# Kernel optimization log

Hardware: AMD Instinct MI355X
Metric: run time of the kernel (lower is better)

Reference implementation:

```python
import jax, jax.numpy as jnp
import numpy as np

SR = 44100
N_BINS = 84
BPO = 12
FMIN = 32.7
HOP = 1024


def _config():
    # Static CQT geometry (mirrors ICQT.__init__)
    Q = 1.0 / (2.0 ** (1.0 / BPO) - 1.0)
    freqs = FMIN * 2.0 ** (np.arange(N_BINS) / BPO)
    wlens = np.round(Q * SR / freqs).astype(np.int64)  # per-bin window lengths (ragged)
    return freqs, wlens


def setup_inputs() -> dict:
    key = jax.random.key(0)
    # complex CQT stacked as (nb_samples, nb_channels, n_bins, n_frames, 2)
    X = jax.random.normal(key, (4, 2, N_BINS, 256, 2), dtype=jnp.float32)
    return {"X": X}


def reference(X):
    freqs, wlens = _config()
    max_wl = int(wlens.max())
    nb_s, nb_c, n_bins, n_frames, _ = X.shape
    # default length in ICQT.forward when length is None
    length = (n_frames - 1) * HOP + max_wl

    Xf = X.reshape(-1, n_bins, n_frames, 2)
    c = (Xf[..., 0] + 1j * Xf[..., 1]).astype(jnp.complex64)  # view_as_complex
    B = c.shape[0]

    starts = np.arange(n_frames) * HOP  # static frame start times
    out = jnp.zeros((B, length), jnp.float32)
    norm_np = np.zeros(length, np.float32)  # norm is input-independent -> static numpy

    for k in range(n_bins):  # fixed structural loop over ragged bins
        L = int(wlens[k])
        t = np.arange(L)
        # torch.hann_window(L) (periodic)
        win = (0.5 - 0.5 * np.cos(2.0 * np.pi * t / L)).astype(np.float32)
        omega = 2.0 * np.pi * float(freqs[k]) / SR
        # exp(+1j*omega*t) * window, fused into one basis vector
        basis = jnp.asarray((np.exp(1j * omega * t) * win).astype(np.complex64))
        # frames: (B, n_frames, L) = outer product of per-frame coeff and basis
        frames = c[:, k, :, None] * basis[None, None, :]
        # vectorized overlap-add scatter (duplicate indices accumulate)
        idx = (starts[:, None] + t[None, :]).reshape(-1)  # (n_frames*L,)
        out = out.at[:, idx].add(jnp.real(frames).reshape(B, -1))
        np.add.at(norm_np, idx, np.tile(win * win, n_frames))

    norm = jnp.asarray(np.where(norm_np > 1e-10, norm_np, 1.0).astype(np.float32))
    out = out / norm[None, :]
    return out.reshape(nb_s, nb_c, -1)
```

## Files before the change

kernel.cpp:

```cpp
#include <hip/hip_runtime.h>
#include <hip/hip_fp16.h>
#include <cmath>

#define NBINS   84
#define NFRAMES 256
#define HOP     1024
#define NB      8
#define KP      960
#define KPH     (KP/2)
#define GBLK    278
#define MROWS   (GBLK*NB)
#define MPAD    2240
#define SD      23

#define BM      64
#define BN      32

#define BT_BLOCKS  1920
#define A_BLOCKS   4200
#define S_BLOCKS   184
#define ALL_BLOCKS (BT_BLOCKS + A_BLOCKS + S_BLOCKS)

typedef _Float16 f16x8 __attribute__((ext_vector_type(8)));
typedef float    f32x4 __attribute__((ext_vector_type(4)));

struct alignas(16) CqtArgs {
    unsigned short ct[KP];
    int   wl[NBINS];
    float omega[NBINS];
    float invL[NBINS];
    int   Ktot;
};

__global__ __launch_bounds__(256)
void build_all(unsigned short* __restrict__ Am, unsigned short* __restrict__ Bt,
               float* __restrict__ S, const float2* __restrict__ X2, CqtArgs a) {
    const int blk = blockIdx.x;
    const int tid = threadIdx.x;
    const float TWOPI = 6.28318530717958647692f;

    if (blk < BT_BLOCKS) {
        const int idx = blk * 256 + tid;
        const int r   = idx / KPH;
        const int j   = idx - r * KPH;
        unsigned int pack = 0;
        const unsigned short rec = a.ct[2 * j];
        if (rec != 0xFFFFu) {
            const int k = rec & 0x7F, d = (rec >> 7) & 0x1F;
            const int t = (d << 10) + r;
            if (t < a.wl[k]) {
                const float tf = (float)t;
                const float w  = 0.5f - 0.5f * cosf(TWOPI * tf * a.invL[k]);
                float s, c;
                sincosf(a.omega[k] * tf, &s, &c);
                pack = (unsigned int)__half_as_ushort(__float2half(c * w))
                     | ((unsigned int)__half_as_ushort(__float2half(s * w)) << 16);
            }
        }
        *(unsigned int*)(Bt + (size_t)r * KP + 2 * j) = pack;
    } else if (blk < BT_BLOCKS + A_BLOCKS) {
        const int idx = (blk - BT_BLOCKS) * 256 + tid;
        const int row = idx / KPH;
        const int j   = idx - row * KPH;
        unsigned int pack = 0;
        const unsigned short rec = a.ct[2 * j];
        if (row < MROWS && rec != 0xFFFFu) {
            const int k = rec & 0x7F, d = (rec >> 7) & 0x1F;
            const int g = row >> 3, b = row & 7;
            const int f = g - d;
            if (f >= 0 && f < NFRAMES) {
                const float2 x = X2[((size_t)b * NBINS + k) * NFRAMES + f];
                pack = (unsigned int)__half_as_ushort(__float2half(x.x))
                     | ((unsigned int)__half_as_ushort(__float2half(-x.y)) << 16);
            }
        }
        *(unsigned int*)(Am + (size_t)row * KP + 2 * j) = pack;
    } else {
        const int gid = (blk - BT_BLOCKS - A_BLOCKS) * 256 + tid;
        const int t   = gid >> 1;
        const int h   = gid & 1;
        float sum = 0.f;
        const int k0 = h * (NBINS / 2);
        for (int k = k0; k < k0 + NBINS / 2; ++k) {
            if (t >= a.wl[k]) break;
            const float w = 0.5f - 0.5f * cosf(TWOPI * (float)t * a.invL[k]);
            sum += w * w;
        }
        const float tot = sum + __shfl_xor(sum, 1, 64);
        if (h == 0) S[t] = tot;
    }
}

__device__ __forceinline__ float inv_norm(const float* __restrict__ S, int g, int ncol) {
    if (g >= GBLK) return 1.0f;
    const int lo = (g > NFRAMES - 1) ? (g - (NFRAMES - 1)) : 0;
    const int hi = g < (SD - 1) ? g : (SD - 1);
    float s = 0.f;
#pragma unroll
    for (int d = 0; d < SD; ++d) {
        const float v = S[(d << 10) + ncol];
        s += (d >= lo && d <= hi) ? v : 0.0f;
    }
    return (s > 1e-10f) ? 1.0f / s : 1.0f;
}

__global__ __launch_bounds__(256)
void gemm_icqt(const unsigned short* __restrict__ Am, const unsigned short* __restrict__ Bt,
               const float* __restrict__ S, float* __restrict__ out, int length) {
    __shared__ __align__(16) char lds[12288];
    const int tid = threadIdx.x;
    const int l   = tid & 63;
    const int wid = tid >> 6;
    const int wm  = wid >> 1, wn = wid & 1;
    const int bm  = blockIdx.x, bn = blockIdx.y;

    const int q0 = tid,      q1 = tid + 256;
    const int r0 = q0 >> 3,  c0 = q0 & 7, s0 = c0 ^ (r0 & 7);
    const int r1 = q1 >> 3,  c1 = q1 & 7, s1 = c1 ^ (r1 & 7);
    const int r2 = tid >> 3, c2 = tid & 7, s2 = c2 ^ (r2 & 7);

    const char* gA0 = (const char*)Am + ((size_t)(bm * BM + r0) * KP + s0 * 8) * 2;
    const char* gA1 = (const char*)Am + ((size_t)(bm * BM + r1) * KP + s1 * 8) * 2;
    const char* gB0 = (const char*)Bt + ((size_t)(bn * BN + r2) * KP + s2 * 8) * 2;
    char* lA = lds;
    char* lB = lds + 8192;

    f32x4 acc0 = {0.f,0.f,0.f,0.f}, acc1 = {0.f,0.f,0.f,0.f};

    f16x8 ra0 = *(const f16x8*)(gA0);
    f16x8 ra1 = *(const f16x8*)(gA1);
    f16x8 rb  = *(const f16x8*)(gB0);

    const int arow0 = wm * 32 + (l & 15), arow1 = arow0 + 16;
    const int brow  = wn * 16 + (l & 15);
    const int kq = l >> 4;

    for (int kk = 0; kk < KP; kk += 64) {
        __syncthreads();
        *(f16x8*)(lA + q0 * 16) = ra0;
        *(f16x8*)(lA + q1 * 16) = ra1;
        *(f16x8*)(lB + tid * 16) = rb;
        __syncthreads();
        if (kk + 64 < KP) {
            ra0 = *(const f16x8*)(gA0 + (kk + 64) * 2);
            ra1 = *(const f16x8*)(gA1 + (kk + 64) * 2);
            rb  = *(const f16x8*)(gB0 + (kk + 64) * 2);
        }
#pragma unroll
        for (int ks = 0; ks < 2; ++ks) {
            const int kb = ks * 4 + kq;
            f16x8 a0 = *(const f16x8*)(lA + arow0 * 128 + ((kb ^ (arow0 & 7)) << 4));
            f16x8 a1 = *(const f16x8*)(lA + arow1 * 128 + ((kb ^ (arow1 & 7)) << 4));
            f16x8 b0 = *(const f16x8*)(lB + brow  * 128 + ((kb ^ (brow  & 7)) << 4));
            acc0 = __builtin_amdgcn_mfma_f32_16x16x32_f16(a0, b0, acc0, 0, 0, 0);
            acc1 = __builtin_amdgcn_mfma_f32_16x16x32_f16(a1, b0, acc1, 0, 0, 0);
        }
    }

    const int mbase = bm * BM + wm * 32;
    const int ncol  = bn * BN + wn * 16 + (l & 15);
    const int g0    = (mbase >> 3) + (kq >> 1);
    const float inv0 = inv_norm(S, g0,     ncol);
    const float inv1 = inv_norm(S, g0 + 2, ncol);

#pragma unroll
    for (int mi = 0; mi < 2; ++mi) {
        const f32x4 v    = mi ? acc1 : acc0;
        const float invv = mi ? inv1 : inv0;
#pragma unroll
        for (int reg = 0; reg < 4; ++reg) {
            const int mrow = mbase + mi * 16 + kq * 4 + reg;
            if (mrow < MROWS) {
                const int g = mrow >> 3, b = mrow & 7;
                const int p = (g << 10) + ncol;
                if (p < length)
                    out[(size_t)b * length + p] = v[reg] * invv;
            }
        }
    }
}

__global__ void icqt_gather_fallback(const float* __restrict__ X, float* __restrict__ out,
                                     CqtArgs a, int length) {
    const int p = blockIdx.x * blockDim.x + threadIdx.x;
    if (p >= length) return;
    float acc[NB];
#pragma unroll
    for (int b = 0; b < NB; ++b) acc[b] = 0.0f;
    float nrm = 0.0f;
    int fhi = p >> 10;
    if (fhi > NFRAMES - 1) fhi = NFRAMES - 1;
    const float2* X2 = reinterpret_cast<const float2*>(X);
    for (int k = 0; k < NBINS; ++k) {
        const int L = a.wl[k];
        int flo = (p - L + HOP) >> 10;
        if (flo < 0) flo = 0;
        for (int f = flo; f <= fhi; ++f) {
            const int t = p - (f << 10);
            if (t < L) {
                float tf = (float)t;
                float ang = a.omega[k] * tf;
                float s = sinf(ang), c = cosf(ang);
                float w = 0.5f - 0.5f * cosf(6.28318530717958647692f * tf * a.invL[k]);
                float bre = c * w, bim = s * w;
                nrm += w * w;
                const int base = k * NFRAMES + f;
#pragma unroll
                for (int b = 0; b < NB; ++b) {
                    float2 cv = X2[(size_t)b * (NBINS * NFRAMES) + base];
                    acc[b] += cv.x * bre - cv.y * bim;
                }
            }
        }
    }
    const float inv = 1.0f / ((nrm > 1e-10f) ? nrm : 1.0f);
#pragma unroll
    for (int b = 0; b < NB; ++b)
        out[(size_t)b * length + p] = acc[b] * inv;
}

extern "C" void kernel_launch(void* const* d_in, const int* in_sizes, int n_in,
                              void* d_out, int out_size, void* d_ws, size_t ws_size,
                              hipStream_t stream) {
    CqtArgs a;
    int cb[NBINS];
    const double SR = 44100.0;
    const double Q  = 1.0 / (std::exp2(1.0 / 12.0) - 1.0);
    int Ktot = 0;
    for (int k = 0; k < NBINS; ++k) {
        double f = 32.7 * std::exp2((double)k / 12.0);
        int L = (int)std::nearbyint(Q * SR / f);
        a.wl[k]    = L;
        cb[k]      = Ktot;
        a.omega[k] = (float)(2.0 * 3.14159265358979323846 * f / SR);
        a.invL[k]  = (float)(1.0 / (double)L);
        Ktot += 2 * ((L + 1023) / 1024);
    }
    a.Ktot = Ktot;
    for (int col = 0; col < KP; ++col) a.ct[col] = 0xFFFF;
    if (Ktot <= KP) {
        for (int k = 0; k < NBINS; ++k) {
            const int D2 = 2 * ((a.wl[k] + 1023) / 1024);
            for (int j = 0; j < D2; ++j)
                a.ct[cb[k] + j] = (unsigned short)(k | ((j >> 1) << 7) | ((j & 1) << 12));
        }
    }

    const int length = out_size / NB;
    const float* X = (const float*)d_in[0];
    float* out     = (float*)d_out;

    const size_t offA = 0;
    const size_t szA  = (size_t)MPAD * KP * 2;
    const size_t offB = offA + szA;
    const size_t szB  = (size_t)1024 * KP * 2;
    const size_t offS = offB + szB;
    const size_t szS  = (size_t)SD * 1024 * 4;
    const size_t need = offS + szS;

    if (Ktot > KP || a.wl[0] > SD * 1024 || ws_size < need) {
        const int blocks = (length + 255) / 256;
        icqt_gather_fallback<<<blocks, 256, 0, stream>>>(X, out, a, length);
        return;
    }

    unsigned short* Am = (unsigned short*)((char*)d_ws + offA);
    unsigned short* Bt = (unsigned short*)((char*)d_ws + offB);
    float*          S  = (float*)((char*)d_ws + offS);

    build_all<<<dim3(ALL_BLOCKS), 256, 0, stream>>>(Am, Bt, S, (const float2*)X, a);
    gemm_icqt<<<dim3(MPAD / BM, 1024 / BN), 256, 0, stream>>>(Am, Bt, S, out, length);
}
```

Before: 47.06 us.

## Double-buffer GEMM K-loop with direct global-to-LDS loads and swizzled block order

Replaces the register-staged single LDS buffer in the GEMM with two LDS buffers filled by global_load_lds instructions, using vmcnt waits and raw barriers so the next K-tile load overlaps the MFMA work. It also flattens the 2D grid into a 1D grid and remaps block IDs so neighbouring blocks share tiles, aiming for better L2 reuse. The LDS footprint doubles, which may lower occupancy. The hand-placed waitcnt and barrier ordering is fragile, and it relies on the direct-to-LDS writes landing in the same XOR-swizzled layout as before.

```diff
diff --git a/kernel.cpp b/kernel.cpp
--- a/kernel.cpp
+++ b/kernel.cpp
@@ -15,6 +15,8 @@
 
 #define BM      64
 #define BN      32
+#define NT      (KP/64)
+#define TILEB   12288
 
 #define BT_BLOCKS  1920
 #define A_BLOCKS   4200
@@ -23,6 +25,14 @@
 
 typedef _Float16 f16x8 __attribute__((ext_vector_type(8)));
 typedef float    f32x4 __attribute__((ext_vector_type(4)));
+
+#define VMCNT(N) asm volatile("s_waitcnt vmcnt(" #N ")" ::: "memory")
+
+__device__ __forceinline__ void gload_lds16(const void* g, void* l) {
+    __builtin_amdgcn_global_load_lds(
+        (__attribute__((address_space(1))) void*)(g),
+        (__attribute__((address_space(3))) void*)(l), 16, 0, 0);
+}
 
 struct alignas(16) CqtArgs {
     unsigned short ct[KP];
@@ -107,12 +117,16 @@
 __global__ __launch_bounds__(256)
 void gemm_icqt(const unsigned short* __restrict__ Am, const unsigned short* __restrict__ Bt,
                const float* __restrict__ S, float* __restrict__ out, int length) {
-    __shared__ __align__(16) char lds[12288];
+    __shared__ __align__(16) char lds[2 * TILEB];
     const int tid = threadIdx.x;
     const int l   = tid & 63;
     const int wid = tid >> 6;
     const int wm  = wid >> 1, wn = wid & 1;
-    const int bm  = blockIdx.x, bn = blockIdx.y;
+
+    const int bid = blockIdx.x;
+    const int swz = (bid & 7) * 140 + (bid >> 3);
+    const int bm  = swz >> 5;
+    const int bn  = swz & 31;
 
     const int q0 = tid,      q1 = tid + 256;
     const int r0 = q0 >> 3,  c0 = q0 & 7, s0 = c0 ^ (r0 & 7);
@@ -122,38 +136,45 @@
     const char* gA0 = (const char*)Am + ((size_t)(bm * BM + r0) * KP + s0 * 8) * 2;
     const char* gA1 = (const char*)Am + ((size_t)(bm * BM + r1) * KP + s1 * 8) * 2;
     const char* gB0 = (const char*)Bt + ((size_t)(bn * BN + r2) * KP + s2 * 8) * 2;
-    char* lA = lds;
-    char* lB = lds + 8192;
 
     f32x4 acc0 = {0.f,0.f,0.f,0.f}, acc1 = {0.f,0.f,0.f,0.f};
-
-    f16x8 ra0 = *(const f16x8*)(gA0);
-    f16x8 ra1 = *(const f16x8*)(gA1);
-    f16x8 rb  = *(const f16x8*)(gB0);
 
     const int arow0 = wm * 32 + (l & 15), arow1 = arow0 + 16;
     const int brow  = wn * 16 + (l & 15);
     const int kq = l >> 4;
 
-    for (int kk = 0; kk < KP; kk += 64) {
-        __syncthreads();
-        *(f16x8*)(lA + q0 * 16) = ra0;
-        *(f16x8*)(lA + q1 * 16) = ra1;
-        *(f16x8*)(lB + tid * 16) = rb;
-        __syncthreads();
-        if (kk + 64 < KP) {
-            ra0 = *(const f16x8*)(gA0 + (kk + 64) * 2);
-            ra1 = *(const f16x8*)(gA1 + (kk + 64) * 2);
-            rb  = *(const f16x8*)(gB0 + (kk + 64) * 2);
-        }
+    {
+        char* bA = lds;            char* bB = lds + 8192;
+        gload_lds16(gA0,       bA + tid * 16);
+        gload_lds16(gA1,       bA + 4096 + tid * 16);
+        gload_lds16(gB0,       bB + tid * 16);
+        char* cA = lds + TILEB;    char* cB = cA + 8192;
+        gload_lds16(gA0 + 128, cA + tid * 16);
+        gload_lds16(gA1 + 128, cA + 4096 + tid * 16);
+        gload_lds16(gB0 + 128, cB + tid * 16);
+    }
+
+#pragma unroll
+    for (int t = 0; t < NT; ++t) {
+        char* bA = lds + (t & 1) * TILEB;
+        char* bB = bA + 8192;
+        if (t + 1 < NT) { VMCNT(3); } else { VMCNT(0); }
+        __builtin_amdgcn_s_barrier();
 #pragma unroll
         for (int ks = 0; ks < 2; ++ks) {
             const int kb = ks * 4 + kq;
-            f16x8 a0 = *(const f16x8*)(lA + arow0 * 128 + ((kb ^ (arow0 & 7)) << 4));
-            f16x8 a1 = *(const f16x8*)(lA + arow1 * 128 + ((kb ^ (arow1 & 7)) << 4));
-            f16x8 b0 = *(const f16x8*)(lB + brow  * 128 + ((kb ^ (brow  & 7)) << 4));
+            f16x8 a0 = *(const f16x8*)(bA + arow0 * 128 + ((kb ^ (arow0 & 7)) << 4));
+            f16x8 a1 = *(const f16x8*)(bA + arow1 * 128 + ((kb ^ (arow1 & 7)) << 4));
+            f16x8 b0 = *(const f16x8*)(bB + brow  * 128 + ((kb ^ (brow  & 7)) << 4));
             acc0 = __builtin_amdgcn_mfma_f32_16x16x32_f16(a0, b0, acc0, 0, 0, 0);
             acc1 = __builtin_amdgcn_mfma_f32_16x16x32_f16(a1, b0, acc1, 0, 0, 0);
+        }
+        if (t + 2 < NT) {
+            __builtin_amdgcn_s_barrier();
+            const int off = (t + 2) * 128;
+            gload_lds16(gA0 + off, bA + tid * 16);
+            gload_lds16(gA1 + off, bA + 4096 + tid * 16);
+            gload_lds16(gB0 + off, bB + tid * 16);
         }
     }
 
@@ -269,5 +290,5 @@
     float*          S  = (float*)((char*)d_ws + offS);
 
     build_all<<<dim3(ALL_BLOCKS), 256, 0, stream>>>(Am, Bt, S, (const float2*)X, a);
-    gemm_icqt<<<dim3(MPAD / BM, 1024 / BN), 256, 0, stream>>>(Am, Bt, S, out, length);
-}
+    gemm_icqt<<<dim3((MPAD / BM) * (1024 / BN)), 256, 0, stream>>>(Am, Bt, S, out, length);
+}
```

Result: faster. 43.37 us (-7.8%).
